# Optimization experiments

Hardware: AMD Instinct MI355X
Metric: run time of the kernel (lower is better)

Reference implementation:

```python
import jax, jax.numpy as jnp
import numpy as np

B, S, H = 2, 2048, 4096
NH, NKV, HD = 32, 8, 128
N_REP = NH // NKV
SCALING = HD ** -0.5


def rotate_half(x):
    x1, x2 = x[..., : HD // 2], x[..., HD // 2 :]
    return jnp.concatenate((-x2, x1), axis=-1)


def setup_inputs() -> dict:
    key = jax.random.key(0)
    ks = jax.random.split(key, 8)
    hidden_states = jax.random.normal(ks[0], (B, S, H), dtype=jnp.float32)
    # RoPE tables computed as in Llama (deterministic, realistic values)
    inv_freq = 1.0 / (10000.0 ** (jnp.arange(0, HD, 2, dtype=jnp.float32) / HD))
    t = jnp.arange(S, dtype=jnp.float32)
    freqs = jnp.einsum('s,d->sd', t, inv_freq)
    emb = jnp.concatenate((freqs, freqs), axis=-1)  # [S, HD]
    cos = jnp.broadcast_to(jnp.cos(emb)[None], (B, S, HD))
    sin = jnp.broadcast_to(jnp.sin(emb)[None], (B, S, HD))
    # additive causal mask [B,1,S,S]
    causal = jnp.where(jnp.tril(jnp.ones((S, S), dtype=bool)), 0.0, -1e9).astype(jnp.float32)
    attention_mask = jnp.broadcast_to(causal[None, None], (B, 1, S, S))
    std = 0.02
    Wq = jax.random.normal(ks[1], (NH * HD, H), dtype=jnp.float32) * std
    Wk = jax.random.normal(ks[2], (NKV * HD, H), dtype=jnp.float32) * std
    Wv = jax.random.normal(ks[3], (NKV * HD, H), dtype=jnp.float32) * std
    Wo = jax.random.normal(ks[4], (H, NH * HD), dtype=jnp.float32) * std
    return dict(hidden_states=hidden_states, cos=cos, sin=sin,
                attention_mask=attention_mask, Wq=Wq, Wk=Wk, Wv=Wv, Wo=Wo)


def reference(hidden_states, cos, sin, attention_mask, Wq, Wk, Wv, Wo):
    b, s, _ = hidden_states.shape
    # projections (torch Linear: x @ W.T), split into heads -> [B, nH, S, HD]
    q = (hidden_states @ Wq.T).reshape(b, s, NH, HD).transpose(0, 2, 1, 3)
    k = (hidden_states @ Wk.T).reshape(b, s, NKV, HD).transpose(0, 2, 1, 3)
    v = (hidden_states @ Wv.T).reshape(b, s, NKV, HD).transpose(0, 2, 1, 3)
    # RoPE: cos/sin [B,S,HD] -> [B,1,S,HD]
    c, sn = cos[:, None], sin[:, None]
    q = q * c + rotate_half(q) * sn
    k = k * c + rotate_half(k) * sn
    # GQA: repeat kv heads
    k = jnp.repeat(k, N_REP, axis=1)
    v = jnp.repeat(v, N_REP, axis=1)
    scores = jnp.einsum('bhqd,bhkd->bhqk', q, k) * SCALING + attention_mask
    attn = jax.nn.softmax(scores.astype(jnp.float32), axis=-1).astype(q.dtype)
    out = jnp.einsum('bhqk,bhkd->bhqd', attn, v)
    out = out.transpose(0, 2, 1, 3).reshape(b, s, NH * HD)
    return out @ Wo.T
```

## Files before the change

kernel.cpp:

```cpp
#include <hip/hip_runtime.h>
#include <stdint.h>

typedef unsigned short u16;
typedef __attribute__((ext_vector_type(8))) short short8;
typedef __attribute__((ext_vector_type(4))) float f32x4;
typedef __attribute__((ext_vector_type(16))) float f32x16;
typedef __attribute__((ext_vector_type(4))) u16 u16x4;

static constexpr float SCALE = 0.08838834764831845f;
static constexpr float QSCALE = 0.12752459769642898f;

__device__ __forceinline__ u16 f2bf(float f) {
    union { float f; unsigned u; } x; x.f = f;
    unsigned r = x.u + 0x7fffu + ((x.u >> 16) & 1u);
    return (u16)(r >> 16);
}
__device__ __forceinline__ float bf2f(u16 b) {
    union { unsigned u; float f; } x; x.u = ((unsigned)b) << 16;
    return x.f;
}
__device__ __forceinline__ unsigned cvt_pk_bf16(float lo, float hi_) {
    unsigned r;
    asm("v_cvt_pk_bf16_f32 %0, %1, %2" : "=v"(r) : "v"(lo), "v"(hi_));
    return r;
}

__global__ __launch_bounds__(256) void convert5_kernel(const float* __restrict__ s0, const float* __restrict__ s1,
                                                       const float* __restrict__ s2, const float* __restrict__ s3,
                                                       const float* __restrict__ s4,
                                                       u16* __restrict__ d0, u16* __restrict__ d1,
                                                       u16* __restrict__ d2, u16* __restrict__ d3,
                                                       u16* __restrict__ d4) {
    const int V0 = 4194304, V1 = 8388608, V2 = 9437184, V3 = 10485760, V4 = 14680064;
    const int stride = gridDim.x * blockDim.x;
    for (int i = blockIdx.x * blockDim.x + threadIdx.x; i < V4; i += stride) {
        const float* sp; u16* dp; int off;
        if (i < V0)      { sp = s0; dp = d0; off = i; }
        else if (i < V1) { sp = s1; dp = d1; off = i - V0; }
        else if (i < V2) { sp = s2; dp = d2; off = i - V1; }
        else if (i < V3) { sp = s3; dp = d3; off = i - V2; }
        else             { sp = s4; dp = d4; off = i - V3; }
        float4 v = *reinterpret_cast<const float4*>(sp + (size_t)off * 4);
        u16x4 o;
        o.x = f2bf(v.x); o.y = f2bf(v.y); o.z = f2bf(v.z); o.w = f2bf(v.w);
        *reinterpret_cast<u16x4*>(dp + (size_t)off * 4) = o;
    }
}

__global__ __launch_bounds__(256) void gemm_kv(const u16* __restrict__ A,
                                               const u16* __restrict__ Bk,
                                               const u16* __restrict__ Bv,
                                               u16* __restrict__ Ck,
                                               u16* __restrict__ Cvt) {
    constexpr int K = 4096, N = 1024, BK = 64;
    __shared__ u16 sA[128 * BK];
    __shared__ u16 sB[128 * BK];
    const int tid = threadIdx.x;
    const int wid = tid >> 6, lane = tid & 63;
    const int lrow = lane & 15, lgrp = lane >> 4;

    int bid = blockIdx.x;
    { const int cpx = 512 >> 3; bid = (bid & 7) * cpx + (bid >> 3); }
    const bool isV = bid >= 256;
    const int b2 = bid & 255;
    const int row0 = (b2 >> 3) * 128, col0 = (b2 & 7) * 128;
    const u16* __restrict__ B = isV ? Bv : Bk;
    const int wr = (wid >> 1) * 64, wc = (wid & 1) * 64;

    f32x4 acc[4][4] = {};

    const int NT = K / BK;
    for (int kt = 0; kt < NT; ++kt) {
        const int k0 = kt * BK;
        __syncthreads();
        #pragma unroll
        for (int rnd = 0; rnd < 4; ++rnd) {
            const int eoff = (rnd * 256 + tid) * 8;
            const int r = eoff >> 6, c = eoff & 63;
            const int gc = c ^ ((r & 7) << 3);
            const int ldsoff = rnd * 2048 + wid * 512;
            __builtin_amdgcn_global_load_lds(
                (const __attribute__((address_space(1))) void*)(A + (size_t)(row0 + r) * K + k0 + gc),
                (__attribute__((address_space(3))) void*)(&sA[ldsoff]), 16, 0, 0);
            __builtin_amdgcn_global_load_lds(
                (const __attribute__((address_space(1))) void*)(B + (size_t)(col0 + r) * K + k0 + gc),
                (__attribute__((address_space(3))) void*)(&sB[ldsoff]), 16, 0, 0);
        }
        __syncthreads();
        #pragma unroll
        for (int kk = 0; kk < 2; ++kk) {
            const int koff = kk * 32 + lgrp * 8;
            short8 af[4], bfr[4];
            #pragma unroll
            for (int m = 0; m < 4; ++m) {
                const int rr = wr + m * 16 + lrow;
                af[m] = *(const short8*)&sA[rr * BK + (koff ^ ((rr & 7) << 3))];
            }
            #pragma unroll
            for (int n = 0; n < 4; ++n) {
                const int rr = wc + n * 16 + lrow;
                bfr[n] = *(const short8*)&sB[rr * BK + (koff ^ ((rr & 7) << 3))];
            }
            #pragma unroll
            for (int m = 0; m < 4; ++m)
                #pragma unroll
                for (int n = 0; n < 4; ++n)
                    acc[m][n] = __builtin_amdgcn_mfma_f32_16x16x32_bf16(af[m], bfr[n], acc[m][n], 0, 0, 0);
        }
    }

    const int orow = row0 + wr + lgrp * 4;
    const int ocol = col0 + wc + lrow;
    if (!isV) {
        #pragma unroll
        for (int m = 0; m < 4; ++m)
            #pragma unroll
            for (int n = 0; n < 4; ++n)
                #pragma unroll
                for (int r = 0; r < 4; ++r)
                    Ck[(size_t)(orow + m * 16 + r) * N + ocol + n * 16] = f2bf(acc[m][n][r]);
    } else {
        #pragma unroll
        for (int m = 0; m < 4; ++m)
            #pragma unroll
            for (int n = 0; n < 4; ++n) {
                u16x4 pk;
                pk.x = f2bf(acc[m][n][0]); pk.y = f2bf(acc[m][n][1]);
                pk.z = f2bf(acc[m][n][2]); pk.w = f2bf(acc[m][n][3]);
                *(u16x4*)&Cvt[(size_t)(ocol + n * 16) * 4096 + orow + m * 16] = pk;
            }
    }
}

template<int OUT_MODE>
__global__ __launch_bounds__(512, 2) void gemm256v3(const u16* __restrict__ A,
                                                    const u16* __restrict__ B,
                                                    void* __restrict__ Cv,
                                                    int M, int N, int K) {
    __shared__ u16 sA[2][2][256 * 32];
    __shared__ u16 sB[2][2][256 * 32];
    const int tid = threadIdx.x;
    const int wid = tid >> 6, lane = tid & 63;
    const int lrow = lane & 15, lgrp = lane >> 4;

    const int nbn = N >> 8;
    const int total = (M >> 8) * nbn;
    int bid = blockIdx.x;
    if ((total & 7) == 0) { const int cpx = total >> 3; bid = (bid & 7) * cpx + (bid >> 3); }
    const int row0 = (bid / nbn) * 256, col0 = (bid % nbn) * 256;
    const int wr = (wid >> 2) * 128, wc = (wid & 3) * 64;

    f32x4 acc[8][4] = {};

    const int rS0 = wid * 32 + (lane >> 2);
    const int uS = lane & 3;

    auto stageA = [&](int nb, int kt, int kkh) {
        const int k0 = kt * 64 + kkh * 32;
        #pragma unroll
        for (int g = 0; g < 2; ++g) {
            const int r = rS0 + g * 16;
            const int cs = k0 + ((uS ^ ((r >> 1) & 3)) << 3);
            __builtin_amdgcn_global_load_lds(
                (const __attribute__((address_space(1))) void*)(A + (size_t)(row0 + r) * K + cs),
                (__attribute__((address_space(3))) void*)(&sA[nb][kkh][(wid * 32 + g * 16) * 32]), 16, 0, 0);
        }
    };
    auto stageB = [&](int nb, int kt, int kkh) {
        const int k0 = kt * 64 + kkh * 32;
        #pragma unroll
        for (int g = 0; g < 2; ++g) {
            const int r = rS0 + g * 16;
            const int cs = k0 + ((uS ^ ((r >> 1) & 3)) << 3);
            __builtin_amdgcn_global_load_lds(
                (const __attribute__((address_space(1))) void*)(B + (size_t)(col0 + r) * K + cs),
                (__attribute__((address_space(3))) void*)(&sB[nb][kkh][(wid * 32 + g * 16) * 32]), 16, 0, 0);
        }
    };

    auto rdA = [&](int buf, int kkh, int fr) -> short8 {
        const int r = wr + fr * 16 + lrow;
        return *(const short8*)&sA[buf][kkh][r * 32 + ((lgrp ^ ((r >> 1) & 3)) << 3)];
    };
    auto rdB = [&](int buf, int kkh, int fc) -> short8 {
        const int r = wc + fc * 16 + lrow;
        return *(const short8*)&sB[buf][kkh][r * 32 + ((lgrp ^ ((r >> 1) & 3)) << 3)];
    };

    const int NK = K >> 6;
    stageA(0, 0, 0); stageB(0, 0, 0); stageA(0, 0, 1); stageB(0, 0, 1);
    asm volatile("s_waitcnt vmcnt(4)" ::: "memory");
    __builtin_amdgcn_s_barrier();
    __builtin_amdgcn_sched_barrier(0);

    for (int kt = 0; kt < NK; ++kt) {
        const int buf = kt & 1, nb = buf ^ 1;
        const bool st = (kt + 1 < NK);
        short8 a[4], b[4], a2[4];

        #pragma unroll
        for (int fr = 0; fr < 4; ++fr) a[fr] = rdA(buf, 0, fr);
        #pragma unroll
        for (int fc = 0; fc < 4; ++fc) b[fc] = rdB(buf, 0, fc);
        if (st) stageA(nb, kt + 1, 0);
        asm volatile("s_waitcnt lgkmcnt(0)" ::: "memory");
        __builtin_amdgcn_sched_barrier(0);
        __builtin_amdgcn_s_setprio(1);
        #pragma unroll
        for (int fr = 0; fr < 4; ++fr)
            #pragma unroll
            for (int fc = 0; fc < 4; ++fc)
                acc[fr][fc] = __builtin_amdgcn_mfma_f32_16x16x32_bf16(a[fr], b[fc], acc[fr][fc], 0, 0, 0);
        __builtin_amdgcn_s_setprio(0);

        #pragma unroll
        for (int fr = 0; fr < 4; ++fr) a2[fr] = rdA(buf, 0, fr + 4);
        if (st) stageB(nb, kt + 1, 0);
        asm volatile("s_waitcnt lgkmcnt(0)" ::: "memory");
        __builtin_amdgcn_sched_barrier(0);
        __builtin_amdgcn_s_setprio(1);
        #pragma unroll
        for (int fr = 0; fr < 4; ++fr)
            #pragma unroll
            for (int fc = 0; fc < 4; ++fc)
                acc[fr + 4][fc] = __builtin_amdgcn_mfma_f32_16x16x32_bf16(a2[fr], b[fc], acc[fr + 4][fc], 0, 0, 0);
        __builtin_amdgcn_s_setprio(0);
        if (st) { asm volatile("s_waitcnt vmcnt(4)" ::: "memory"); }
        else    { asm volatile("s_waitcnt vmcnt(0)" ::: "memory"); }
        __builtin_amdgcn_s_barrier();
        __builtin_amdgcn_sched_barrier(0);

        #pragma unroll
        for (int fr = 0; fr < 4; ++fr) a[fr] = rdA(buf, 1, fr);
        #pragma unroll
        for (int fc = 0; fc < 4; ++fc) b[fc] = rdB(buf, 1, fc);
        if (st) stageA(nb, kt + 1, 1);
        asm volatile("s_waitcnt lgkmcnt(0)" ::: "memory");
        __builtin_amdgcn_sched_barrier(0);
        __builtin_amdgcn_s_setprio(1);
        #pragma unroll
        for (int fr = 0; fr < 4; ++fr)
            #pragma unroll
            for (int fc = 0; fc < 4; ++fc)
                acc[fr][fc] = __builtin_amdgcn_mfma_f32_16x16x32_bf16(a[fr], b[fc], acc[fr][fc], 0, 0, 0);
        __builtin_amdgcn_s_setprio(0);

        #pragma unroll
        for (int fr = 0; fr < 4; ++fr) a2[fr] = rdA(buf, 1, fr + 4);
        if (st) stageB(nb, kt + 1, 1);
        asm volatile("s_waitcnt lgkmcnt(0)" ::: "memory");
        __builtin_amdgcn_sched_barrier(0);
        __builtin_amdgcn_s_setprio(1);
        #pragma unroll
        for (int fr = 0; fr < 4; ++fr)
            #pragma unroll
            for (int fc = 0; fc < 4; ++fc)
                acc[fr + 4][fc] = __builtin_amdgcn_mfma_f32_16x16x32_bf16(a2[fr], b[fc], acc[fr + 4][fc], 0, 0, 0);
        __builtin_amdgcn_s_setprio(0);
        if (st) { asm volatile("s_waitcnt vmcnt(4)" ::: "memory"); }
        __builtin_amdgcn_s_barrier();
        __builtin_amdgcn_sched_barrier(0);
    }

    const int orow = row0 + wr + lgrp * 4;
    const int ocol = col0 + wc + lrow;
    if (OUT_MODE == 2) {
        float* C = (float*)Cv;
        #pragma unroll
        for (int m = 0; m < 8; ++m)
            #pragma unroll
            for (int n = 0; n < 4; ++n)
                #pragma unroll
                for (int r = 0; r < 4; ++r)
                    C[(size_t)(orow + m * 16 + r) * N + ocol + n * 16] = acc[m][n][r];
    } else {
        u16* C = (u16*)Cv;
        #pragma unroll
        for (int m = 0; m < 8; ++m)
            #pragma unroll
            for (int n = 0; n < 4; ++n)
                #pragma unroll
                for (int r = 0; r < 4; ++r)
                    C[(size_t)(orow + m * 16 + r) * N + ocol + n * 16] = f2bf(acc[m][n][r]);
    }
}

template<int NHEADS>
__global__ __launch_bounds__(256) void rope_kernel(u16* __restrict__ X,
                                                   const float* __restrict__ cosb,
                                                   const float* __restrict__ sinb,
                                                   float scale) {
    constexpr int LH = (NHEADS == 32) ? 5 : 3;
    const int total = 2 * 2048 * NHEADS * 64;
    const int stride = gridDim.x * blockDim.x;
    for (int i = blockIdx.x * blockDim.x + threadIdx.x; i < total; i += stride) {
        const int d = i & 63;
        const int h = (i >> 6) & (NHEADS - 1);
        const int rs = i >> (6 + LH);
        const size_t base = (size_t)rs * (NHEADS * 128) + h * 128 + d;
        const float c = cosb[rs * 128 + d] * scale;
        const float sn = sinb[rs * 128 + d] * scale;
        const float x1 = bf2f(X[base]);
        const float x2 = bf2f(X[base + 64]);
        X[base] = f2bf(x1 * c - x2 * sn);
        X[base + 64] = f2bf(x2 * c + x1 * sn);
    }
}

__global__ __launch_bounds__(512, 2) void attn_kernel(const u16* __restrict__ Q,
                                                      const u16* __restrict__ K,
                                                      const u16* __restrict__ Vt,
                                                      u16* __restrict__ AO,
                                                      const float* __restrict__ cosp,
                                                      const float* __restrict__ sinp) {
    __shared__ u16 sK[2][64 * 128];
    __shared__ u16 sV[2][128 * 64];
    const int tid = threadIdx.x;
    const int wid = tid >> 6, lane = tid & 63;
    const int l31 = lane & 31, hi = lane >> 5;

    const int gg = blockIdx.x >> 6;
    const int bx = (gg < 4) ? gg : 11 - gg;
    const int rem = blockIdx.x & 63;
    const int h = rem >> 1;
    const int b = rem & 1;
    const int hkv = h >> 2;
    const int rs0 = b * 2048;
    const int q0 = bx * 256;
    const int qw = q0 + wid * 32;
    const int q_lane = qw + l31;

    short8 qf[8];
    {
        const u16* qb = Q + (size_t)(rs0 + q_lane) * 4096 + h * 128 + hi * 8;
        #pragma unroll
        for (int f = 0; f < 8; ++f) qf[f] = *(const short8*)(qb + f * 16);
        const float* cb = cosp + (size_t)(rs0 + q_lane) * 128 + hi * 8;
        const float* sb = sinp + (size_t)(rs0 + q_lane) * 128 + hi * 8;
        #pragma unroll
        for (int f = 0; f < 4; ++f) {
            float4 c0 = *(const float4*)(cb + f * 16);
            float4 c1 = *(const float4*)(cb + f * 16 + 4);
            float4 s0 = *(const float4*)(sb + f * 16);
            float4 s1 = *(const float4*)(sb + f * 16 + 4);
            const float cc[8] = {c0.x, c0.y, c0.z, c0.w, c1.x, c1.y, c1.z, c1.w};
            const float ss[8] = {s0.x, s0.y, s0.z, s0.w, s1.x, s1.y, s1.z, s1.w};
            #pragma unroll
            for (int j = 0; j < 8; ++j) {
                const float x1 = bf2f((u16)qf[f][j]);
                const float x2 = bf2f((u16)qf[f + 4][j]);
                qf[f][j]     = (short)f2bf((x1 * cc[j] - x2 * ss[j]) * QSCALE);
                qf[f + 4][j] = (short)f2bf((x2 * cc[j] + x1 * ss[j]) * QSCALE);
            }
        }
    }

    f32x16 accO[4] = {};
    float m_c = -1e30f, l_c = 0.f;

    auto stage = [&](int bf, int t) {
        const int kv0 = t * 64;
        #pragma unroll
        for (int rnd = 0; rnd < 2; ++rnd) {
            {
                const int e = rnd * 4096 + tid * 8;
                const int r = e >> 7, c = e & 127;
                const int cs = c ^ ((r & 15) << 3);
                __builtin_amdgcn_global_load_lds(
                    (const __attribute__((address_space(1))) void*)(K + (size_t)(rs0 + kv0 + r) * 1024 + hkv * 128 + cs),
                    (__attribute__((address_space(3))) void*)(&sK[bf][rnd * 4096 + wid * 512]), 16, 0, 0);
            }
            {
                const int e = rnd * 4096 + tid * 8;
                const int r = e >> 6, c = e & 63;
                const int cs = c ^ ((r & 7) << 3);
                __builtin_amdgcn_global_load_lds(
                    (const __attribute__((address_space(1))) void*)(Vt + (size_t)(hkv * 128 + r) * 4096 + rs0 + kv0 + cs),
                    (__attribute__((address_space(3))) void*)(&sV[bf][rnd * 4096 + wid * 512]), 16, 0, 0);
            }
        }
    };

    const int NT = 4 * (bx + 1);
    stage(0, 0);
    __syncthreads();
    int buf = 0;

    for (int t = 0; t < NT; ++t) {
        if (t + 1 < NT) stage(buf ^ 1, t + 1);
        const int kv0 = t * 64;

        if (kv0 <= qw + 31) {
            f32x16 sc[2] = {};
            #pragma unroll
            for (int f = 0; f < 8; ++f) {
                const int col = f * 16 + hi * 8;
                const int r0 = l31, r1 = 32 + l31;
                short8 k0 = *(const short8*)&sK[buf][r0 * 128 + (col ^ ((r0 & 15) << 3))];
                short8 k1 = *(const short8*)&sK[buf][r1 * 128 + (col ^ ((r1 & 15) << 3))];
                sc[0] = __builtin_amdgcn_mfma_f32_32x32x16_bf16(k0, qf[f], sc[0], 0, 0, 0);
                sc[1] = __builtin_amdgcn_mfma_f32_32x32x16_bf16(k1, qf[f], sc[1], 0, 0, 0);
            }

            if (kv0 + 63 > q_lane) {
                #pragma unroll
                for (int blk = 0; blk < 2; ++blk)
                    #pragma unroll
                    for (int r = 0; r < 16; ++r) {
                        const int kv_abs = kv0 + blk * 32 + ((r & 3) + 8 * (r >> 2) + 4 * hi);
                        if (kv_abs > q_lane) sc[blk][r] = -1e30f;
                    }
            }

            float mx = sc[0][0];
            #pragma unroll
            for (int blk = 0; blk < 2; ++blk)
                #pragma unroll
                for (int r = 0; r < 16; ++r) mx = fmaxf(mx, sc[blk][r]);
            mx = fmaxf(mx, __shfl_xor(mx, 32));

            if (!__all(mx <= m_c + 8.0f)) {
                const float sclf = __builtin_amdgcn_exp2f(m_c - mx);
                m_c = mx;
                l_c *= sclf;
                float sclq[16];
                #pragma unroll
                for (int r = 0; r < 16; ++r)
                    sclq[r] = __shfl(sclf, (r & 3) + 8 * (r >> 2) + 4 * hi);
                #pragma unroll
                for (int d4 = 0; d4 < 4; ++d4)
                    #pragma unroll
                    for (int r = 0; r < 16; ++r) accO[d4][r] *= sclq[r];
            }
            float ssum = 0.f;
            #pragma unroll
            for (int blk = 0; blk < 2; ++blk)
                #pragma unroll
                for (int r = 0; r < 16; ++r) {
                    const float p = __builtin_amdgcn_exp2f(sc[blk][r] - m_c);
                    sc[blk][r] = p;
                    ssum += p;
                }
            ssum += __shfl_xor(ssum, 32);
            l_c += ssum;

            #pragma unroll
            for (int blk = 0; blk < 2; ++blk) {
                #pragma unroll
                for (int tt = 0; tt < 2; ++tt) {
                    const unsigned cv00 = cvt_pk_bf16(sc[blk][8 * tt + 0], sc[blk][8 * tt + 1]);
                    const unsigned cv01 = cvt_pk_bf16(sc[blk][8 * tt + 2], sc[blk][8 * tt + 3]);
                    const unsigned cv10 = cvt_pk_bf16(sc[blk][8 * tt + 4], sc[blk][8 * tt + 5]);
                    const unsigned cv11 = cvt_pk_bf16(sc[blk][8 * tt + 6], sc[blk][8 * tt + 7]);
                    const unsigned s00 = __shfl_xor(cv00, 32);
                    const unsigned s01 = __shfl_xor(cv01, 32);
                    const unsigned s10 = __shfl_xor(cv10, 32);
                    const unsigned s11 = __shfl_xor(cv11, 32);
                    union { unsigned w[4]; short8 v; } pa;
                    pa.w[0] = hi ? s10 : cv00;
                    pa.w[1] = hi ? s11 : cv01;
                    pa.w[2] = hi ? cv10 : s00;
                    pa.w[3] = hi ? cv11 : s01;
                    const int kvb = blk * 32 + tt * 16 + hi * 8;
                    #pragma unroll
                    for (int d4 = 0; d4 < 4; ++d4) {
                        const int vr = d4 * 32 + l31;
                        short8 vf = *(const short8*)&sV[buf][vr * 64 + (kvb ^ ((vr & 7) << 3))];
                        accO[d4] = __builtin_amdgcn_mfma_f32_32x32x16_bf16(pa.v, vf, accO[d4], 0, 0, 0);
                    }
                }
            }
        }
        __syncthreads();
        buf ^= 1;
    }

    const float invl = 1.0f / l_c;
    float invq[16];
    #pragma unroll
    for (int r = 0; r < 16; ++r)
        invq[r] = __shfl(invl, (r & 3) + 8 * (r >> 2) + 4 * hi);
    #pragma unroll
    for (int d4 = 0; d4 < 4; ++d4)
        #pragma unroll
        for (int r = 0; r < 16; ++r) {
            const int q = qw + (r & 3) + 8 * (r >> 2) + 4 * hi;
            AO[(size_t)(rs0 + q) * 4096 + h * 128 + d4 * 32 + l31] = f2bf(accO[d4][r] * invq[r]);
        }
}

extern "C" void kernel_launch(void* const* d_in, const int* in_sizes, int n_in,
                              void* d_out, int out_size, void* d_ws, size_t ws_size,
                              hipStream_t stream) {
    const float* hs   = (const float*)d_in[0];
    const float* cosp = (const float*)d_in[1];
    const float* sinp = (const float*)d_in[2];
    const float* Wq = (const float*)d_in[4];
    const float* Wk = (const float*)d_in[5];
    const float* Wv = (const float*)d_in[6];
    const float* Wo = (const float*)d_in[7];

    u16* Xb = (u16*)d_out;
    u16* Qb = (u16*)d_out + 16777216;
    char* w = (char*)d_ws;
    u16* Wqb = (u16*)w; w += 33554432;
    u16* Wkb = (u16*)w; w += 8388608;
    u16* Wvb = (u16*)w; w += 8388608;
    u16* Wob = (u16*)w; w += 33554432;
    u16* Kb  = (u16*)w; w += 8388608;
    u16* Vtb = (u16*)w; w += 8388608;
    u16* AOb = (u16*)w; w += 33554432;

    convert5_kernel<<<4096, 256, 0, stream>>>(hs, Wq, Wk, Wv, Wo, Xb, Wqb, Wkb, Wvb, Wob);

    gemm256v3<0><<<256, 512, 0, stream>>>(Xb, Wqb, Qb, 4096, 4096, 4096);
    gemm_kv<<<512, 256, 0, stream>>>(Xb, Wkb, Wvb, Kb, Vtb);

    rope_kernel<8><<<1024, 256, 0, stream>>>(Kb, cosp, sinp, 1.0f);

    attn_kernel<<<512, 512, 0, stream>>>(Qb, Kb, Vtb, AOb, cosp, sinp);

    gemm256v3<2><<<256, 512, 0, stream>>>(AOb, Wob, (float*)d_out, 4096, 4096, 4096);
}
```

Measured before the change: 507.4 us.

## Load GEMM B operand directly from global into registers, dropping LDS staging

The 256x256 GEMM now keeps only the A tile in shared memory and has each wave fetch its B fragments straight from global memory into registers, double-buffered one k-tile ahead. This halves LDS footprint and removes the LDS write/read traffic and one barrier per half-tile for B. In exchange, B is fetched redundantly by the two wave rows (each B row is loaded twice), global loads are less coalesced (16-byte strided reads across rows of K), and register pressure rises with 16 short8 B registers held live.

After: 1.022 ms. 101% more time.

```diff
diff --git a/kernel.cpp b/kernel.cpp
--- a/kernel.cpp
+++ b/kernel.cpp
@@ -133,12 +133,11 @@
 }
 
 template<int OUT_MODE>
-__global__ __launch_bounds__(512, 2) void gemm256v3(const u16* __restrict__ A,
+__global__ __launch_bounds__(512, 2) void gemm256v4(const u16* __restrict__ A,
                                                     const u16* __restrict__ B,
                                                     void* __restrict__ Cv,
                                                     int M, int N, int K) {
     __shared__ u16 sA[2][2][256 * 32];
-    __shared__ u16 sB[2][2][256 * 32];
     const int tid = threadIdx.x;
     const int wid = tid >> 6, lane = tid & 63;
     const int lrow = lane & 15, lgrp = lane >> 4;
@@ -166,43 +165,37 @@
                 (__attribute__((address_space(3))) void*)(&sA[nb][kkh][(wid * 32 + g * 16) * 32]), 16, 0, 0);
         }
     };
-    auto stageB = [&](int nb, int kt, int kkh) {
-        const int k0 = kt * 64 + kkh * 32;
-        #pragma unroll
-        for (int g = 0; g < 2; ++g) {
-            const int r = rS0 + g * 16;
-            const int cs = k0 + ((uS ^ ((r >> 1) & 3)) << 3);
-            __builtin_amdgcn_global_load_lds(
-                (const __attribute__((address_space(1))) void*)(B + (size_t)(col0 + r) * K + cs),
-                (__attribute__((address_space(3))) void*)(&sB[nb][kkh][(wid * 32 + g * 16) * 32]), 16, 0, 0);
-        }
-    };
-
     auto rdA = [&](int buf, int kkh, int fr) -> short8 {
         const int r = wr + fr * 16 + lrow;
         return *(const short8*)&sA[buf][kkh][r * 32 + ((lgrp ^ ((r >> 1) & 3)) << 3)];
     };
-    auto rdB = [&](int buf, int kkh, int fc) -> short8 {
-        const int r = wc + fc * 16 + lrow;
-        return *(const short8*)&sB[buf][kkh][r * 32 + ((lgrp ^ ((r >> 1) & 3)) << 3)];
+    const u16* __restrict__ Bb = B + (size_t)(col0 + wc + lrow) * K + lgrp * 8;
+    auto ldB = [&](int kt, int kkh, int fc) -> short8 {
+        return *(const short8*)(Bb + (size_t)(fc * 16) * K + kt * 64 + kkh * 32);
     };
 
     const int NK = K >> 6;
-    stageA(0, 0, 0); stageB(0, 0, 0); stageA(0, 0, 1); stageB(0, 0, 1);
-    asm volatile("s_waitcnt vmcnt(4)" ::: "memory");
-    __builtin_amdgcn_s_barrier();
-    __builtin_amdgcn_sched_barrier(0);
-
-    for (int kt = 0; kt < NK; ++kt) {
-        const int buf = kt & 1, nb = buf ^ 1;
-        const bool st = (kt + 1 < NK);
-        short8 a[4], b[4], a2[4];
+    stageA(0, 0, 0); stageA(0, 0, 1);
+    short8 b0[8], b1[8];
+    #pragma unroll
+    for (int kkh = 0; kkh < 2; ++kkh)
+        #pragma unroll
+        for (int fc = 0; fc < 4; ++fc) b0[kkh * 4 + fc] = ldB(0, kkh, fc);
+    __syncthreads();
+
+    auto tile = [&](int t, short8 (&cur)[8], short8 (&nxt)[8]) {
+        const int buf = t & 1, nb = buf ^ 1;
+        const bool st = (t + 1 < NK);
+        short8 a[4];
 
         #pragma unroll
         for (int fr = 0; fr < 4; ++fr) a[fr] = rdA(buf, 0, fr);
-        #pragma unroll
-        for (int fc = 0; fc < 4; ++fc) b[fc] = rdB(buf, 0, fc);
-        if (st) stageA(nb, kt + 1, 0);
+        if (st) {
+            #pragma unroll
+            for (int kkh = 0; kkh < 2; ++kkh)
+                #pragma unroll
+                for (int fc = 0; fc < 4; ++fc) nxt[kkh * 4 + fc] = ldB(t + 1, kkh, fc);
+        }
         asm volatile("s_waitcnt lgkmcnt(0)" ::: "memory");
         __builtin_amdgcn_sched_barrier(0);
         __builtin_amdgcn_s_setprio(1);
@@ -210,12 +203,12 @@
         for (int fr = 0; fr < 4; ++fr)
             #pragma unroll
             for (int fc = 0; fc < 4; ++fc)
-                acc[fr][fc] = __builtin_amdgcn_mfma_f32_16x16x32_bf16(a[fr], b[fc], acc[fr][fc], 0, 0, 0);
+                acc[fr][fc] = __builtin_amdgcn_mfma_f32_16x16x32_bf16(a[fr], cur[fc], acc[fr][fc], 0, 0, 0);
         __builtin_amdgcn_s_setprio(0);
 
         #pragma unroll
-        for (int fr = 0; fr < 4; ++fr) a2[fr] = rdA(buf, 0, fr + 4);
-        if (st) stageB(nb, kt + 1, 0);
+        for (int fr = 0; fr < 4; ++fr) a[fr] = rdA(buf, 0, fr + 4);
+        if (st) stageA(nb, t + 1, 0);
         asm volatile("s_waitcnt lgkmcnt(0)" ::: "memory");
         __builtin_amdgcn_sched_barrier(0);
         __builtin_amdgcn_s_setprio(1);
@@ -223,18 +216,12 @@
         for (int fr = 0; fr < 4; ++fr)
             #pragma unroll
             for (int fc = 0; fc < 4; ++fc)
-                acc[fr + 4][fc] = __builtin_amdgcn_mfma_f32_16x16x32_bf16(a2[fr], b[fc], acc[fr + 4][fc], 0, 0, 0);
+                acc[fr + 4][fc] = __builtin_amdgcn_mfma_f32_16x16x32_bf16(a[fr], cur[fc], acc[fr + 4][fc], 0, 0, 0);
         __builtin_amdgcn_s_setprio(0);
-        if (st) { asm volatile("s_waitcnt vmcnt(4)" ::: "memory"); }
-        else    { asm volatile("s_waitcnt vmcnt(0)" ::: "memory"); }
-        __builtin_amdgcn_s_barrier();
-        __builtin_amdgcn_sched_barrier(0);
 
         #pragma unroll
         for (int fr = 0; fr < 4; ++fr) a[fr] = rdA(buf, 1, fr);
-        #pragma unroll
-        for (int fc = 0; fc < 4; ++fc) b[fc] = rdB(buf, 1, fc);
-        if (st) stageA(nb, kt + 1, 1);
+        if (st) stageA(nb, t + 1, 1);
         asm volatile("s_waitcnt lgkmcnt(0)" ::: "memory");
         __builtin_amdgcn_sched_barrier(0);
         __builtin_amdgcn_s_setprio(1);
@@ -242,12 +229,11 @@
         for (int fr = 0; fr < 4; ++fr)
             #pragma unroll
             for (int fc = 0; fc < 4; ++fc)
-                acc[fr][fc] = __builtin_amdgcn_mfma_f32_16x16x32_bf16(a[fr], b[fc], acc[fr][fc], 0, 0, 0);
+                acc[fr][fc] = __builtin_amdgcn_mfma_f32_16x16x32_bf16(a[fr], cur[4 + fc], acc[fr][fc], 0, 0, 0);
         __builtin_amdgcn_s_setprio(0);
 
         #pragma unroll
-        for (int fr = 0; fr < 4; ++fr) a2[fr] = rdA(buf, 1, fr + 4);
-        if (st) stageB(nb, kt + 1, 1);
+        for (int fr = 0; fr < 4; ++fr) a[fr] = rdA(buf, 1, fr + 4);
         asm volatile("s_waitcnt lgkmcnt(0)" ::: "memory");
         __builtin_amdgcn_sched_barrier(0);
         __builtin_amdgcn_s_setprio(1);
@@ -255,11 +241,14 @@
         for (int fr = 0; fr < 4; ++fr)
             #pragma unroll
             for (int fc = 0; fc < 4; ++fc)
-                acc[fr + 4][fc] = __builtin_amdgcn_mfma_f32_16x16x32_bf16(a2[fr], b[fc], acc[fr + 4][fc], 0, 0, 0);
+                acc[fr + 4][fc] = __builtin_amdgcn_mfma_f32_16x16x32_bf16(a[fr], cur[4 + fc], acc[fr + 4][fc], 0, 0, 0);
         __builtin_amdgcn_s_setprio(0);
-        if (st) { asm volatile("s_waitcnt vmcnt(4)" ::: "memory"); }
-        __builtin_amdgcn_s_barrier();
-        __builtin_amdgcn_sched_barrier(0);
+        __syncthreads();
+    };
+
+    for (int t2 = 0; t2 < NK; t2 += 2) {
+        tile(t2, b0, b1);
+        tile(t2 + 1, b1, b0);
     }
 
     const int orow = row0 + wr + lgrp * 4;
@@ -513,12 +502,12 @@
 
     convert5_kernel<<<4096, 256, 0, stream>>>(hs, Wq, Wk, Wv, Wo, Xb, Wqb, Wkb, Wvb, Wob);
 
-    gemm256v3<0><<<256, 512, 0, stream>>>(Xb, Wqb, Qb, 4096, 4096, 4096);
+    gemm256v4<0><<<256, 512, 0, stream>>>(Xb, Wqb, Qb, 4096, 4096, 4096);
     gemm_kv<<<512, 256, 0, stream>>>(Xb, Wkb, Wvb, Kb, Vtb);
 
     rope_kernel<8><<<1024, 256, 0, stream>>>(Kb, cosp, sinp, 1.0f);
 
     attn_kernel<<<512, 512, 0, stream>>>(Qb, Kb, Vtb, AOb, cosp, sinp);
 
-    gemm256v3<2><<<256, 512, 0, stream>>>(AOb, Wob, (float*)d_out, 4096, 4096, 4096);
-}
+    gemm256v4<2><<<256, 512, 0, stream>>>(AOb, Wob, (float*)d_out, 4096, 4096, 4096);
+}
```
